# Kernel tuning notes

Hardware: AMD Instinct MI355X
Metric: run time of the kernel (lower is better)

## Reference

```python
import jax, jax.numpy as jnp
import numpy as np

SEQ_LEN = 600
N_CLASSES = 5
P = 6  # max_ar_order


def setup_inputs() -> dict:
    key = jax.random.key(0)
    N = 32768
    x = jax.random.normal(key, (N, SEQ_LEN), dtype=jnp.float32)
    return {"x": x}


def reference(x):
    N = x.shape[0]
    T_out = SEQ_LEN - P
    # Lag matrix: X_lag[:, t, k] = x[:, P-1-k + t]  -> [N, T_out, P]
    X_lag = jnp.stack([x[:, P - 1 - k:SEQ_LEN - 1 - k] for k in range(P)], axis=-1)
    y = x[:, P:]  # [N, T_out]
    ones = jnp.ones((N, T_out, 1), dtype=x.dtype)
    D = jnp.concatenate([ones, X_lag], axis=-1)  # [N, T_out, P+1]
    # Least squares via normal equations (tiny (P+1)x(P+1) batched solve)
    G = jnp.einsum('ntk,ntl->nkl', D, D)        # [N, P+1, P+1]
    b = jnp.einsum('ntk,nt->nk', D, y)          # [N, P+1]
    w = jnp.linalg.solve(G, b[..., None])[..., 0]  # [N, P+1]
    y_hat_valid = jnp.einsum('ntk,nk->nt', D, w)   # [N, T_out]
    x_hat = jnp.zeros((N, SEQ_LEN), dtype=x.dtype).at[:, P:].set(y_hat_valid)
    ar_coeffs = w[:, 1:]  # [N, P]
    coeffs = jnp.broadcast_to(ar_coeffs[:, None, :], (N, SEQ_LEN, P))
    # zero the first P time steps
    t_mask = (jnp.arange(SEQ_LEN) >= P).astype(x.dtype)[None, :, None]
    coeffs = coeffs * t_mask
    p_logits = jnp.zeros((N, N_CLASSES), dtype=x.dtype)
    p_hard = jnp.zeros((N,), dtype=jnp.int32)
    return (coeffs, p_logits, p_hard, x_hat)
```

## Files before the change

### kernel.cpp

```cpp
#include <hip/hip_runtime.h>

#define SEQ 600
#define PP 6
#define TOUT 594

__global__ __launch_bounds__(256) void ar_fit_kernel(
    const float* __restrict__ x,
    float* __restrict__ coeffs,
    float* __restrict__ x_hat,
    int N)
{
    __shared__ __align__(16) float sxr[4][608];
    __shared__ float4 spat[4][3];

    const int wave = threadIdx.x >> 6;
    const int lane = threadIdx.x & 63;
    const int row  = (blockIdx.x << 2) + wave;
    const bool live = (row < N);

    if (live) {
        const float4* xr = reinterpret_cast<const float4*>(x + (size_t)row * SEQ);
        float4* s4 = reinterpret_cast<float4*>(sxr[wave]);
        for (int i = lane; i < SEQ / 4; i += 64) s4[i] = xr[i];
        if (lane < 8) sxr[wave][SEQ + lane] = 0.0f;
    }
    __syncthreads();

    const float* sx = sxr[wave];
    float w[7];

    if (live) {
        float S = 0.f;
        float Q[7] = {0.f, 0.f, 0.f, 0.f, 0.f, 0.f, 0.f};
        for (int i = lane; i < SEQ; i += 64) {
            float x0 = sx[i];
            S += x0;
            #pragma unroll
            for (int d = 0; d < 7; ++d) Q[d] += x0 * sx[i + d];
        }
        #pragma unroll
        for (int m = 1; m < 64; m <<= 1) {
            S += __shfl_xor(S, m, 64);
            #pragma unroll
            for (int d = 0; d < 7; ++d) Q[d] += __shfl_xor(Q[d], m, 64);
        }

        float pre[8], suf[8];
        pre[0] = 0.f; suf[0] = 0.f;
        #pragma unroll
        for (int c = 1; c < 8; ++c) {
            pre[c] = pre[c - 1] + sx[c - 1];
            suf[c] = suf[c - 1] + sx[SEQ - c];
        }

        float M[7][7];
        float rhs[7];
        M[0][0] = (float)TOUT;
        #pragma unroll
        for (int k = 0; k < 6; ++k) {
            float v = S - pre[5 - k] - suf[k + 1];
            M[0][k + 1] = v; M[k + 1][0] = v;
        }
        #pragma unroll
        for (int k = 0; k < 6; ++k) {
            #pragma unroll
            for (int l = k; l < 6; ++l) {
                const int a = 5 - l, d = l - k;
                float head = 0.f;
                #pragma unroll
                for (int i = 0; i < a; ++i) head += sx[i] * sx[i + d];
                float tail = 0.f;
                #pragma unroll
                for (int i = a + TOUT; i < SEQ; ++i) tail += sx[i] * sx[i + d];
                float v = Q[d] - head - tail;
                M[k + 1][l + 1] = v; M[l + 1][k + 1] = v;
            }
        }
        rhs[0] = S - pre[6];
        #pragma unroll
        for (int k = 0; k < 6; ++k) {
            const int a = 5 - k, d = k + 1;
            float head = 0.f;
            #pragma unroll
            for (int i = 0; i < a; ++i) head += sx[i] * sx[i + d];
            float tail = 0.f;
            #pragma unroll
            for (int i = a + TOUT; i < SEQ; ++i) tail += sx[i] * sx[i + d];
            rhs[k + 1] = Q[d] - head - tail;
        }

        #pragma unroll
        for (int j = 0; j < 7; ++j) {
            float s = M[j][j];
            #pragma unroll
            for (int m = 0; m < j; ++m) s -= M[j][m] * M[j][m];
            float ljj = sqrtf(s);
            M[j][j] = ljj;
            float inv = 1.0f / ljj;
            #pragma unroll
            for (int i2 = j + 1; i2 < 7; ++i2) {
                float s2 = M[i2][j];
                #pragma unroll
                for (int m = 0; m < j; ++m) s2 -= M[i2][m] * M[j][m];
                M[i2][j] = s2 * inv;
            }
        }
        float z[7];
        #pragma unroll
        for (int i2 = 0; i2 < 7; ++i2) {
            float s = rhs[i2];
            #pragma unroll
            for (int m = 0; m < i2; ++m) s -= M[i2][m] * z[m];
            z[i2] = s / M[i2][i2];
        }
        #pragma unroll
        for (int i2 = 6; i2 >= 0; --i2) {
            float s = z[i2];
            #pragma unroll
            for (int m = i2 + 1; m < 7; ++m) s -= M[m][i2] * w[m];
            w[i2] = s / M[i2][i2];
        }

        if (lane == 0) {
            float* p = reinterpret_cast<float*>(spat[wave]);
            #pragma unroll
            for (int m = 0; m < 12; ++m) p[m] = w[1 + (m % 6)];
        }
    }
    __syncthreads();

    if (!live) return;

    {
        float4* crow = reinterpret_cast<float4*>(coeffs + (size_t)row * (SEQ * PP));
        const float4* pw = spat[wave];
        int r = lane % 3;
        for (int i = lane; i < (SEQ * PP) / 4; i += 64) {
            float4 v = pw[r];
            if (i < 9) {
                float* vp = reinterpret_cast<float*>(&v);
                #pragma unroll
                for (int j = 0; j < 4; ++j)
                    if (4 * i + j < PP * PP) vp[j] = 0.f;
            }
            crow[i] = v;
            r = (r == 2) ? 0 : (r + 1);
        }
    }

    {
        float* xh = x_hat + (size_t)row * SEQ;
        for (int e = lane; e < SEQ; e += 64) {
            float v = 0.f;
            if (e >= PP) {
                v = w[0];
                #pragma unroll
                for (int k = 1; k <= 6; ++k) v += w[k] * sx[e - k];
            }
            xh[e] = v;
        }
    }
}

extern "C" void kernel_launch(void* const* d_in, const int* in_sizes, int n_in,
                              void* d_out, int out_size, void* d_ws, size_t ws_size,
                              hipStream_t stream) {
    const float* x = (const float*)d_in[0];
    const int N = in_sizes[0] / SEQ;

    float* out    = (float*)d_out;
    float* coeffs = out;
    float* extra  = out + (size_t)N * SEQ * PP;
    float* x_hat  = extra + (size_t)N * 6;

    hipMemsetAsync(extra, 0, (size_t)N * 6 * sizeof(float), stream);

    dim3 grid((N + 3) / 4), block(256);
    ar_fit_kernel<<<grid, block, 0, stream>>>(x, coeffs, x_hat, N);
}
```

Baseline: 594.2 us.

## Split coefficient broadcast into separate fill kernel and vectorize x_hat stores

The fit kernel now writes the 7 solved weights to a workspace buffer and stores x_hat with float4 writes. A second kernel, with one 256-thread block per row, fills the large coeffs output, so the ~86 MB write is spread over many more threads than one wave per row. This also removes the shared-memory pattern staging and the second block barrier. The costs are an extra launch, a workspace round trip, and the removal of the N%4 bounds guard.

```diff
diff --git a/kernel.cpp b/kernel.cpp
--- a/kernel.cpp
+++ b/kernel.cpp
@@ -6,19 +6,16 @@
 
 __global__ __launch_bounds__(256) void ar_fit_kernel(
     const float* __restrict__ x,
-    float* __restrict__ coeffs,
     float* __restrict__ x_hat,
-    int N)
+    float* __restrict__ wout)
 {
     __shared__ __align__(16) float sxr[4][608];
-    __shared__ float4 spat[4][3];
 
     const int wave = threadIdx.x >> 6;
     const int lane = threadIdx.x & 63;
     const int row  = (blockIdx.x << 2) + wave;
-    const bool live = (row < N);
-
-    if (live) {
+
+    {
         const float4* xr = reinterpret_cast<const float4*>(x + (size_t)row * SEQ);
         float4* s4 = reinterpret_cast<float4*>(sxr[wave]);
         for (int i = lane; i < SEQ / 4; i += 64) s4[i] = xr[i];
@@ -29,136 +26,158 @@
     const float* sx = sxr[wave];
     float w[7];
 
-    if (live) {
-        float S = 0.f;
-        float Q[7] = {0.f, 0.f, 0.f, 0.f, 0.f, 0.f, 0.f};
-        for (int i = lane; i < SEQ; i += 64) {
-            float x0 = sx[i];
-            S += x0;
-            #pragma unroll
-            for (int d = 0; d < 7; ++d) Q[d] += x0 * sx[i + d];
-        }
-        #pragma unroll
-        for (int m = 1; m < 64; m <<= 1) {
-            S += __shfl_xor(S, m, 64);
-            #pragma unroll
-            for (int d = 0; d < 7; ++d) Q[d] += __shfl_xor(Q[d], m, 64);
-        }
-
-        float pre[8], suf[8];
-        pre[0] = 0.f; suf[0] = 0.f;
-        #pragma unroll
-        for (int c = 1; c < 8; ++c) {
-            pre[c] = pre[c - 1] + sx[c - 1];
-            suf[c] = suf[c - 1] + sx[SEQ - c];
-        }
-
-        float M[7][7];
-        float rhs[7];
-        M[0][0] = (float)TOUT;
-        #pragma unroll
-        for (int k = 0; k < 6; ++k) {
-            float v = S - pre[5 - k] - suf[k + 1];
-            M[0][k + 1] = v; M[k + 1][0] = v;
-        }
-        #pragma unroll
-        for (int k = 0; k < 6; ++k) {
-            #pragma unroll
-            for (int l = k; l < 6; ++l) {
-                const int a = 5 - l, d = l - k;
-                float head = 0.f;
-                #pragma unroll
-                for (int i = 0; i < a; ++i) head += sx[i] * sx[i + d];
-                float tail = 0.f;
-                #pragma unroll
-                for (int i = a + TOUT; i < SEQ; ++i) tail += sx[i] * sx[i + d];
-                float v = Q[d] - head - tail;
-                M[k + 1][l + 1] = v; M[l + 1][k + 1] = v;
-            }
-        }
-        rhs[0] = S - pre[6];
-        #pragma unroll
-        for (int k = 0; k < 6; ++k) {
-            const int a = 5 - k, d = k + 1;
+    float S = 0.f;
+    float Q[7] = {0.f, 0.f, 0.f, 0.f, 0.f, 0.f, 0.f};
+    for (int i = lane; i < SEQ; i += 64) {
+        float x0 = sx[i];
+        S += x0;
+        #pragma unroll
+        for (int d = 0; d < 7; ++d) Q[d] += x0 * sx[i + d];
+    }
+    #pragma unroll
+    for (int m = 1; m < 64; m <<= 1) {
+        S += __shfl_xor(S, m, 64);
+        #pragma unroll
+        for (int d = 0; d < 7; ++d) Q[d] += __shfl_xor(Q[d], m, 64);
+    }
+
+    float pre[8], suf[8];
+    pre[0] = 0.f; suf[0] = 0.f;
+    #pragma unroll
+    for (int c = 1; c < 8; ++c) {
+        pre[c] = pre[c - 1] + sx[c - 1];
+        suf[c] = suf[c - 1] + sx[SEQ - c];
+    }
+
+    float M[7][7];
+    float rhs[7];
+    M[0][0] = (float)TOUT;
+    #pragma unroll
+    for (int k = 0; k < 6; ++k) {
+        float v = S - pre[5 - k] - suf[k + 1];
+        M[0][k + 1] = v; M[k + 1][0] = v;
+    }
+    #pragma unroll
+    for (int k = 0; k < 6; ++k) {
+        #pragma unroll
+        for (int l = k; l < 6; ++l) {
+            const int a = 5 - l, d = l - k;
             float head = 0.f;
             #pragma unroll
             for (int i = 0; i < a; ++i) head += sx[i] * sx[i + d];
             float tail = 0.f;
             #pragma unroll
             for (int i = a + TOUT; i < SEQ; ++i) tail += sx[i] * sx[i + d];
-            rhs[k + 1] = Q[d] - head - tail;
-        }
-
-        #pragma unroll
-        for (int j = 0; j < 7; ++j) {
-            float s = M[j][j];
-            #pragma unroll
-            for (int m = 0; m < j; ++m) s -= M[j][m] * M[j][m];
-            float ljj = sqrtf(s);
-            M[j][j] = ljj;
-            float inv = 1.0f / ljj;
-            #pragma unroll
-            for (int i2 = j + 1; i2 < 7; ++i2) {
-                float s2 = M[i2][j];
-                #pragma unroll
-                for (int m = 0; m < j; ++m) s2 -= M[i2][m] * M[j][m];
-                M[i2][j] = s2 * inv;
+            float v = Q[d] - head - tail;
+            M[k + 1][l + 1] = v; M[l + 1][k + 1] = v;
+        }
+    }
+    rhs[0] = S - pre[6];
+    #pragma unroll
+    for (int k = 0; k < 6; ++k) {
+        const int a = 5 - k, d = k + 1;
+        float head = 0.f;
+        #pragma unroll
+        for (int i = 0; i < a; ++i) head += sx[i] * sx[i + d];
+        float tail = 0.f;
+        #pragma unroll
+        for (int i = a + TOUT; i < SEQ; ++i) tail += sx[i] * sx[i + d];
+        rhs[k + 1] = Q[d] - head - tail;
+    }
+
+    #pragma unroll
+    for (int j = 0; j < 7; ++j) {
+        float s = M[j][j];
+        #pragma unroll
+        for (int m = 0; m < j; ++m) s -= M[j][m] * M[j][m];
+        float ljj = sqrtf(s);
+        M[j][j] = ljj;
+        float inv = 1.0f / ljj;
+        #pragma unroll
+        for (int i2 = j + 1; i2 < 7; ++i2) {
+            float s2 = M[i2][j];
+            #pragma unroll
+            for (int m = 0; m < j; ++m) s2 -= M[i2][m] * M[j][m];
+            M[i2][j] = s2 * inv;
+        }
+    }
+    float z[7];
+    #pragma unroll
+    for (int i2 = 0; i2 < 7; ++i2) {
+        float s = rhs[i2];
+        #pragma unroll
+        for (int m = 0; m < i2; ++m) s -= M[i2][m] * z[m];
+        z[i2] = s / M[i2][i2];
+    }
+    #pragma unroll
+    for (int i2 = 6; i2 >= 0; --i2) {
+        float s = z[i2];
+        #pragma unroll
+        for (int m = i2 + 1; m < 7; ++m) s -= M[m][i2] * w[m];
+        w[i2] = s / M[i2][i2];
+    }
+
+    if (lane == 0) {
+        float4* wo = reinterpret_cast<float4*>(wout + (size_t)row * 8);
+        float4 a = make_float4(w[0], w[1], w[2], w[3]);
+        float4 b = make_float4(w[4], w[5], w[6], 0.f);
+        wo[0] = a;
+        wo[1] = b;
+    }
+
+    {
+        float4* xh4 = reinterpret_cast<float4*>(x_hat + (size_t)row * SEQ);
+        for (int i = lane; i < SEQ / 4; i += 64) {
+            float4 v;
+            float* vp = reinterpret_cast<float*>(&v);
+            #pragma unroll
+            for (int c = 0; c < 4; ++c) {
+                int e = 4 * i + c;
+                float p = 0.f;
+                if (e >= PP) {
+                    p = w[0];
+                    #pragma unroll
+                    for (int k = 1; k <= 6; ++k) p += w[k] * sx[e - k];
+                }
+                vp[c] = p;
             }
-        }
-        float z[7];
-        #pragma unroll
-        for (int i2 = 0; i2 < 7; ++i2) {
-            float s = rhs[i2];
-            #pragma unroll
-            for (int m = 0; m < i2; ++m) s -= M[i2][m] * z[m];
-            z[i2] = s / M[i2][i2];
-        }
-        #pragma unroll
-        for (int i2 = 6; i2 >= 0; --i2) {
-            float s = z[i2];
-            #pragma unroll
-            for (int m = i2 + 1; m < 7; ++m) s -= M[m][i2] * w[m];
-            w[i2] = s / M[i2][i2];
-        }
-
-        if (lane == 0) {
-            float* p = reinterpret_cast<float*>(spat[wave]);
-            #pragma unroll
-            for (int m = 0; m < 12; ++m) p[m] = w[1 + (m % 6)];
-        }
-    }
-    __syncthreads();
-
-    if (!live) return;
-
-    {
-        float4* crow = reinterpret_cast<float4*>(coeffs + (size_t)row * (SEQ * PP));
-        const float4* pw = spat[wave];
-        int r = lane % 3;
-        for (int i = lane; i < (SEQ * PP) / 4; i += 64) {
-            float4 v = pw[r];
+            xh4[i] = v;
+        }
+    }
+}
+
+__global__ __launch_bounds__(256) void coeff_fill_kernel(
+    const float* __restrict__ wout,
+    float* __restrict__ coeffs)
+{
+    const int row = blockIdx.x;
+    const int t   = threadIdx.x;
+
+    const float* wr = wout + (size_t)row * 8;
+    const float w1 = wr[1], w2 = wr[2], w3 = wr[3];
+    const float w4 = wr[4], w5 = wr[5], w6 = wr[6];
+
+    const float4 P0 = make_float4(w1, w2, w3, w4);
+    const float4 P1 = make_float4(w5, w6, w1, w2);
+    const float4 P2 = make_float4(w3, w4, w5, w6);
+
+    float4* out = reinterpret_cast<float4*>(coeffs + (size_t)row * (SEQ * PP));
+
+    int r = t % 3;
+    #pragma unroll
+    for (int j = 0; j < 4; ++j) {
+        const int i = t + 256 * j;
+        if (i < (SEQ * PP) / 4) {
+            float4 v = (r == 0) ? P0 : ((r == 1) ? P1 : P2);
             if (i < 9) {
                 float* vp = reinterpret_cast<float*>(&v);
                 #pragma unroll
-                for (int j = 0; j < 4; ++j)
-                    if (4 * i + j < PP * PP) vp[j] = 0.f;
+                for (int c = 0; c < 4; ++c)
+                    if (4 * i + c < PP * PP) vp[c] = 0.f;
             }
-            crow[i] = v;
-            r = (r == 2) ? 0 : (r + 1);
-        }
-    }
-
-    {
-        float* xh = x_hat + (size_t)row * SEQ;
-        for (int e = lane; e < SEQ; e += 64) {
-            float v = 0.f;
-            if (e >= PP) {
-                v = w[0];
-                #pragma unroll
-                for (int k = 1; k <= 6; ++k) v += w[k] * sx[e - k];
-            }
-            xh[e] = v;
-        }
+            out[i] = v;
+        }
+        r = (r == 2) ? 0 : (r + 1);
     }
 }
 
@@ -172,9 +191,10 @@
     float* coeffs = out;
     float* extra  = out + (size_t)N * SEQ * PP;
     float* x_hat  = extra + (size_t)N * 6;
+    float* wbuf   = (float*)d_ws;
 
     hipMemsetAsync(extra, 0, (size_t)N * 6 * sizeof(float), stream);
 
-    dim3 grid((N + 3) / 4), block(256);
-    ar_fit_kernel<<<grid, block, 0, stream>>>(x, coeffs, x_hat, N);
+    ar_fit_kernel<<<dim3(N / 4), dim3(256), 0, stream>>>(x, x_hat, wbuf);
+    coeff_fill_kernel<<<dim3(N), dim3(256), 0, stream>>>(wbuf, coeffs);
 }
```

Result: slower. 613.4 us (+3.2%).
